# Kernel optimization log

Measured on AMD Instinct MI355X. Metric: run time of the kernel, lower is better.

The kernel has to match this reference:

```python
import jax, jax.numpy as jnp
import numpy as np

H = W = 512
P = H * W          # total superpixel member pixels
N_SP = 1024        # number of superpixels


def _conv(x, w, b):
    # x: [N,C,H,W], w: [O,I,3,3] -> [N,O,H,W], SAME padding
    y = jax.lax.conv_general_dilated(
        x, w, window_strides=(1, 1), padding='SAME',
        dimension_numbers=('NCHW', 'OIHW', 'NCHW'))
    return y + b[None, :, None, None]


def _embed(raw, w1, b1, w2, b2, w3, b3):
    h = jax.nn.relu(_conv(raw, w1, b1))
    h = jax.nn.relu(_conv(h, w2, b2))
    return _conv(h, w3, b3)  # [1, 10, H, W]


def setup_inputs() -> dict:
    key = jax.random.key(0)
    ks = jax.random.split(key, 6)
    raw = jax.random.normal(ks[0], (1, 1, H, W), dtype=jnp.float32)
    w1 = jax.random.normal(ks[1], (64, 1, 3, 3), dtype=jnp.float32) * 0.3
    b1 = jnp.zeros((64,), jnp.float32)
    w2 = jax.random.normal(ks[2], (64, 64, 3, 3), dtype=jnp.float32) * 0.05
    b2 = jnp.zeros((64,), jnp.float32)
    w3 = jax.random.normal(ks[3], (10, 64, 3, 3), dtype=jnp.float32) * 0.05
    b3 = jnp.zeros((10,), jnp.float32)
    pix_rc = jax.random.randint(ks[4], (P, 2), 0, H, dtype=jnp.int32)
    seg_ids = jax.random.randint(ks[5], (P,), 0, N_SP, dtype=jnp.int32)
    return {"raw": raw, "w1": w1, "b1": b1, "w2": w2, "b2": b2,
            "w3": w3, "b3": b3, "pix_rc": pix_rc, "seg_ids": seg_ids,
            "n_sp": N_SP}


def reference(raw, w1, b1, w2, b2, w3, b3, pix_rc, seg_ids, n_sp):
    feats = _embed(raw, w1, b1, w2, b2, w3, b3)  # [1, C, H, W]
    f = feats[0]                                  # [C, H, W]
    # gather per-pixel feature vectors: [P, C]
    vals = f[:, pix_rc[:, 0], pix_rc[:, 1]].T
    # scatter-mean over superpixels (= per-sp sum / mass)
    sums = jax.ops.segment_sum(vals, seg_ids, num_segments=n_sp)      # [n_sp, C]
    cnts = jax.ops.segment_sum(jnp.ones((vals.shape[0],), vals.dtype),
                               seg_ids, num_segments=n_sp)            # [n_sp]
    return sums / jnp.maximum(cnts, 1.0)[:, None]
```

## Files before the change

kernel.cpp:

```cpp
#include <hip/hip_runtime.h>

typedef __attribute__((ext_vector_type(8))) short short8;
typedef __attribute__((ext_vector_type(4))) float f32x4;

constexpr int H = 512, W = 512;
constexpr int P = H * W;
constexpr int NSP = 1024;
constexpr int SBLK = 512;
constexpr int FGRP = 16;

__device__ inline unsigned short f2bf(float f) {
  unsigned u = __builtin_bit_cast(unsigned, f);
  unsigned r = (u + 0x7fffu + ((u >> 16) & 1u)) >> 16;
  return (unsigned short)r;
}
__device__ inline float bflo(unsigned u) { return __builtin_bit_cast(float, u << 16); }
__device__ inline float bfhi(unsigned u) { return __builtin_bit_cast(float, u & 0xffff0000u); }

__device__ inline int xcd_swz(int b, int cpx) { return (b & 7) * cpx + (b >> 3); }

__global__ __launch_bounds__(256) void prep_k(const float* __restrict__ w2,
                                              const float* __restrict__ w3,
                                              unsigned short* __restrict__ wt2s,
                                              unsigned short* __restrict__ wt3s) {
  int i = blockIdx.x * 256 + threadIdx.x;
  if (i < 36864) {
    int k = i >> 11;
    int t = (i >> 3) & 255;
    int e = i & 7;
    int r = t >> 2, sp = t & 3, s = sp ^ (r & 3);
    int tap = k >> 1, ic = (k & 1) * 32 + s * 8 + e;
    wt2s[i] = f2bf(w2[r * 576 + ic * 9 + tap]);
  } else if (i < 46080) {
    int j = i - 36864;
    int k = j >> 9;
    int t = (j >> 3) & 63;
    int e = j & 7;
    int r = t >> 2, sp = t & 3, s = sp ^ (r & 3);
    int tap = k >> 1, ic = (k & 1) * 32 + s * 8 + e;
    wt3s[j] = (r < 10) ? f2bf(w3[r * 576 + ic * 9 + tap]) : (unsigned short)0;
  }
}

__global__ __launch_bounds__(512, 4) void conv123_k(const float* __restrict__ raw,
                                                    const float* __restrict__ w1,
                                                    const float* __restrict__ b1,
                                                    const unsigned short* __restrict__ wts2,
                                                    const float* __restrict__ b2,
                                                    const unsigned short* __restrict__ wts3,
                                                    const float* __restrict__ b3,
                                                    unsigned short* __restrict__ feats) {
  constexpr int WCS = 2048;
  __shared__ __align__(16) unsigned short acts[448 * 64];
  __shared__ __align__(16) unsigned short wbuf[3 * WCS];
  __shared__ float rawt[14 * 38];
  int tid = threadIdx.x;
  int lane = tid & 63, wave = tid >> 6;
  int logical = xcd_swz(blockIdx.x, 128);
  int tilex = logical & 15, tiley = logical >> 4;
  int c0 = tilex * 32, r0 = tiley * 8;

  if (tid < 256) {
#pragma unroll
    for (int k0 = 0; k0 < 2; ++k0) {
      const unsigned short* src = wts2 + (size_t)k0 * WCS + tid * 8;
      unsigned short* dstb = wbuf + k0 * WCS + wave * 512;
      __builtin_amdgcn_global_load_lds((const __attribute__((address_space(1))) void*)src,
                                       (__attribute__((address_space(3))) void*)dstb, 16, 0, 0);
    }
  }
  for (int i = tid; i < 532; i += 512) {
    int rr = i / 38, cc = i - rr * 38;
    int gr = r0 + rr - 3, gc = c0 + cc - 3;
    bool ok = ((unsigned)gr < 512u) && ((unsigned)gc < 512u);
    rawt[i] = ok ? raw[gr * 512 + gc] : 0.f;
  }

  int q = lane >> 4, n = lane & 15;
  int og1 = wave & 3;
  short8 a1f;
  {
    short av[8];
#pragma unroll
    for (int e = 0; e < 8; ++e) av[e] = 0;
    int oc = og1 * 16 + n;
    if (q == 0) {
#pragma unroll
      for (int e = 0; e < 8; ++e) av[e] = (short)f2bf(w1[oc * 9 + e]);
    } else if (q == 1) {
      av[0] = (short)f2bf(w1[oc * 9 + 8]);
    }
    a1f = (short8){av[0], av[1], av[2], av[3], av[4], av[5], av[6], av[7]};
  }
  float bb1[4];
#pragma unroll
  for (int r2 = 0; r2 < 4; ++r2) bb1[r2] = b1[og1 * 16 + q * 4 + r2];
  __syncthreads();

  char* actw = (char*)acts;
  int hhalf = wave >> 2;
  for (int i1 = 0; i1 < 14; ++i1) {
    int t = 2 * i1 + hhalf;
    if (t >= 27) break;
    int px = t * 16 + n;
    int py = px / 36, pxc = px - py * 36;
    short bv[8];
#pragma unroll
    for (int e = 0; e < 8; ++e) bv[e] = 0;
    if (q == 0) {
#pragma unroll
      for (int e = 0; e < 8; ++e) {
        int dy = e / 3, dx = e - dy * 3;
        bv[e] = (short)f2bf(rawt[(py + dy) * 38 + pxc + dx]);
      }
    } else if (q == 1) {
      bv[0] = (short)f2bf(rawt[(py + 2) * 38 + pxc + 2]);
    }
    short8 b1f = (short8){bv[0], bv[1], bv[2], bv[3], bv[4], bv[5], bv[6], bv[7]};
    f32x4 d = __builtin_amdgcn_mfma_f32_16x16x32_bf16(a1f, b1f,
                                                       (f32x4){0.f, 0.f, 0.f, 0.f}, 0, 0, 0);
    int gr1 = r0 + py - 2, gc1 = c0 + pxc - 2;
    bool ok1 = ((unsigned)gr1 < 512u) && ((unsigned)gc1 < 512u);
    float o0 = ok1 ? fmaxf(d.x + bb1[0], 0.f) : 0.f;
    float o1 = ok1 ? fmaxf(d.y + bb1[1], 0.f) : 0.f;
    float o2 = ok1 ? fmaxf(d.z + bb1[2], 0.f) : 0.f;
    float o3 = ok1 ? fmaxf(d.w + bb1[3], 0.f) : 0.f;
    unsigned lo = (unsigned)f2bf(o0) | ((unsigned)f2bf(o1) << 16);
    unsigned hi = (unsigned)f2bf(o2) | ((unsigned)f2bf(o3) << 16);
    int wa = px * 128 + ((((og1 * 2 + (q >> 1)) ^ (px & 7)) << 4)) + ((q & 1) << 3);
    *reinterpret_cast<uint2*>(actw + wa) = make_uint2(lo, hi);
  }
  __syncthreads();

  f32x4 acc[4][3];
#pragma unroll
  for (int og = 0; og < 4; ++og)
#pragma unroll
    for (int g = 0; g < 3; ++g) acc[og][g] = (f32x4){0.f, 0.f, 0.f, 0.f};
  const char* actb = (const char*)acts;

#pragma unroll
  for (int k = 0; k < 18; ++k) {
    if (k == 17) {
      asm volatile("s_waitcnt vmcnt(0)" ::: "memory");
    } else {
      asm volatile("s_waitcnt vmcnt(1)" ::: "memory");
    }
    __builtin_amdgcn_sched_barrier(0);
    __builtin_amdgcn_s_barrier();
    __builtin_amdgcn_sched_barrier(0);
    if (k + 2 < 18 && tid < 256) {
      const unsigned short* src = wts2 + (size_t)(k + 2) * WCS + tid * 8;
      unsigned short* dstb = wbuf + ((k + 2) % 3) * WCS + wave * 512;
      __builtin_amdgcn_global_load_lds((const __attribute__((address_space(1))) void*)src,
                                       (__attribute__((address_space(3))) void*)dstb, 16, 0, 0);
    }
    const int tap = k >> 1, kc = k & 1;
    const int kyy = tap / 3, kxx = tap - kyy * 3;
    const char* wb = (const char*)(wbuf + (k % 3) * WCS);
    short8 af[4];
#pragma unroll
    for (int og = 0; og < 4; ++og) {
      int r = og * 16 + n;
      af[og] = *reinterpret_cast<const short8*>(wb + r * 64 + ((q ^ (r & 3)) * 16));
    }
#pragma unroll
    for (int g = 0; g < 3; ++g) {
      int t2 = wave + 8 * g;
      if (t2 < 23) {
        int pl = t2 * 16 + n + kyy * 36 + kxx;
        int addr = pl * 128 + (((kc * 4 + q) ^ (pl & 7)) * 16);
        short8 bf = *reinterpret_cast<const short8*>(actb + addr);
#pragma unroll
        for (int og = 0; og < 4; ++og)
          acc[og][g] = __builtin_amdgcn_mfma_f32_16x16x32_bf16(af[og], bf, acc[og][g], 0, 0, 0);
      }
    }
  }
  __syncthreads();

  if (tid < 64) {
#pragma unroll
    for (int k0 = 0; k0 < 2; ++k0) {
      const unsigned short* src = wts3 + (size_t)k0 * 512 + lane * 8;
      unsigned short* dstb = &wbuf[k0 * 512];
      __builtin_amdgcn_global_load_lds((const __attribute__((address_space(1))) void*)src,
                                       (__attribute__((address_space(3))) void*)dstb, 16, 0, 0);
    }
  }
#pragma unroll
  for (int g = 0; g < 3; ++g) {
    int t2 = wave + 8 * g;
    if (t2 < 23) {
      int px2 = t2 * 16 + n;
#pragma unroll
      for (int og = 0; og < 4; ++og) {
        f32x4 v = acc[og][g];
        float o0 = fmaxf(v.x + b2[og * 16 + q * 4 + 0], 0.f);
        float o1 = fmaxf(v.y + b2[og * 16 + q * 4 + 1], 0.f);
        float o2 = fmaxf(v.z + b2[og * 16 + q * 4 + 2], 0.f);
        float o3 = fmaxf(v.w + b2[og * 16 + q * 4 + 3], 0.f);
        unsigned lo = (unsigned)f2bf(o0) | ((unsigned)f2bf(o1) << 16);
        unsigned hi = (unsigned)f2bf(o2) | ((unsigned)f2bf(o3) << 16);
        int lslot = og * 2 + (q >> 1);
        int wa = px2 * 128 + (((lslot ^ (px2 & 7)) << 4)) + ((q & 1) << 3);
        *reinterpret_cast<uint2*>(actw + wa) = make_uint2(lo, hi);
      }
    }
  }
  __syncthreads();

  f32x4 acc3[2];
#pragma unroll
  for (int g = 0; g < 2; ++g) acc3[g] = (f32x4){0.f, 0.f, 0.f, 0.f};
  const char* wb3 = (const char*)wbuf;

#pragma unroll
  for (int k = 0; k < 18; ++k) {
    if (k == 17) {
      asm volatile("s_waitcnt vmcnt(0)" ::: "memory");
    } else {
      asm volatile("s_waitcnt vmcnt(1)" ::: "memory");
    }
    __builtin_amdgcn_sched_barrier(0);
    __builtin_amdgcn_s_barrier();
    __builtin_amdgcn_sched_barrier(0);
    if (k + 2 < 18 && tid < 64) {
      const unsigned short* src = wts3 + (size_t)(k + 2) * 512 + lane * 8;
      unsigned short* dstb = &wbuf[((k + 2) % 3) * 512];
      __builtin_amdgcn_global_load_lds((const __attribute__((address_space(1))) void*)src,
                                       (__attribute__((address_space(3))) void*)dstb, 16, 0, 0);
    }
    const int tap = k >> 1, kc = k & 1;
    const int kyy = tap / 3, kxx = tap - kyy * 3;
    short8 af = *reinterpret_cast<const short8*>(wb3 + (k % 3) * 1024 + n * 64 + ((q ^ (n & 3)) * 16));
#pragma unroll
    for (int g = 0; g < 2; ++g) {
      int pl = wave * 36 + g * 16 + n + kyy * 36 + kxx;
      int addr = pl * 128 + (((kc * 4 + q) ^ (pl & 7)) * 16);
      short8 bf = *reinterpret_cast<const short8*>(actb + addr);
      acc3[g] = __builtin_amdgcn_mfma_f32_16x16x32_bf16(af, bf, acc3[g], 0, 0, 0);
    }
  }

  __syncthreads();
  char* ob = (char*)acts;
  float bb3[4];
#pragma unroll
  for (int r2 = 0; r2 < 4; ++r2) {
    int oc = q * 4 + r2;
    bb3[r2] = (oc < 10) ? b3[oc] : 0.f;
  }
#pragma unroll
  for (int g = 0; g < 2; ++g) {
    int pl = wave * 32 + g * 16 + n;
    f32x4 v = acc3[g];
    float o0 = v.x + bb3[0], o1 = v.y + bb3[1], o2 = v.z + bb3[2], o3 = v.w + bb3[3];
    if (q < 2) {
      unsigned u0 = (unsigned)f2bf(o0) | ((unsigned)f2bf(o1) << 16);
      unsigned u1 = (unsigned)f2bf(o2) | ((unsigned)f2bf(o3) << 16);
      *reinterpret_cast<uint2*>(ob + pl * 24 + q * 8) = make_uint2(u0, u1);
    } else if (q == 2) {
      *reinterpret_cast<unsigned*>(ob + pl * 24 + 16) =
          (unsigned)f2bf(o0) | ((unsigned)f2bf(o1) << 16);
    }
  }
  __syncthreads();
  char* fb = (char*)feats;
#pragma unroll
  for (int it = 0; it < 3; ++it) {
    int c = it * 512 + tid;
    if (c < 1280) {
      int row = c / 160, wb = c - row * 160;
      int byte = wb * 4;
      int px = byte / 20, off = byte - px * 20;
      unsigned v = *reinterpret_cast<const unsigned*>(ob + (row * 32 + px) * 24 + off);
      size_t gbyte = (((size_t)(r0 + row) * 512) + c0) * 20 + (size_t)byte;
      *reinterpret_cast<unsigned*>(fb + gbyte) = v;
    }
  }
}

__global__ __launch_bounds__(512) void scatter_k(const unsigned short* __restrict__ feats,
                                                 const int* __restrict__ pix_rc,
                                                 const int* __restrict__ seg,
                                                 float* __restrict__ partials) {
  __shared__ float ls[NSP * 10];
  __shared__ float lc[NSP];
  int tid = threadIdx.x;
  for (int i = tid; i < NSP * 10; i += 512) ls[i] = 0.f;
  for (int i = tid; i < NSP; i += 512) lc[i] = 0.f;
  __syncthreads();

  constexpr int PER = P / SBLK;
  int p0 = blockIdx.x * PER;
  for (int p = p0 + tid; p < p0 + PER; p += 512) {
    int r = pix_rc[2 * p], c = pix_rc[2 * p + 1];
    int s = seg[p];
    size_t gpix = (size_t)r * 512 + c;
    const char* fp = (const char*)feats + gpix * 20;
    uint4 a = *reinterpret_cast<const uint4*>(fp);
    unsigned e = *reinterpret_cast<const unsigned*>(fp + 16);
    float v[10];
    v[0] = bflo(a.x); v[1] = bfhi(a.x);
    v[2] = bflo(a.y); v[3] = bfhi(a.y);
    v[4] = bflo(a.z); v[5] = bfhi(a.z);
    v[6] = bflo(a.w); v[7] = bfhi(a.w);
    v[8] = bflo(e);   v[9] = bfhi(e);
#pragma unroll
    for (int ch = 0; ch < 10; ++ch) atomicAdd(&ls[s * 10 + ch], v[ch]);
    atomicAdd(&lc[s], 1.f);
  }
  __syncthreads();

  float* outp = partials + (size_t)blockIdx.x * (NSP * 11);
  for (int i = tid; i < NSP * 10; i += 512) outp[i] = ls[i];
  for (int i = tid; i < NSP; i += 512) outp[NSP * 10 + i] = lc[i];
}

__global__ __launch_bounds__(256) void finA_k(const float* __restrict__ partials,
                                              float* __restrict__ partials2) {
  int g = blockIdx.x / 44;
  int e = (blockIdx.x - g * 44) * 256 + threadIdx.x;
  const float* base = partials + (size_t)(g * 32) * (NSP * 11) + e;
  float s = 0.f;
#pragma unroll 8
  for (int k = 0; k < 32; ++k) s += base[(size_t)k * (NSP * 11)];
  partials2[(size_t)g * (NSP * 11) + e] = s;
}

__global__ __launch_bounds__(256) void finB_k(const float* __restrict__ partials2,
                                              float* __restrict__ out) {
  int i = blockIdx.x * 256 + threadIdx.x;
  if (i >= NSP * 10) return;
  int sp = i / 10;
  float s = 0.f, cnt = 0.f;
#pragma unroll
  for (int g = 0; g < FGRP; ++g) {
    const float* pp = partials2 + (size_t)g * (NSP * 11);
    s += pp[i];
    cnt += pp[NSP * 10 + sp];
  }
  out[i] = s / fmaxf(cnt, 1.f);
}

extern "C" void kernel_launch(void* const* d_in, const int* in_sizes, int n_in,
                              void* d_out, int out_size, void* d_ws, size_t ws_size,
                              hipStream_t stream) {
  const float* raw = (const float*)d_in[0];
  const float* w1  = (const float*)d_in[1];
  const float* b1  = (const float*)d_in[2];
  const float* w2  = (const float*)d_in[3];
  const float* b2  = (const float*)d_in[4];
  const float* w3  = (const float*)d_in[5];
  const float* b3  = (const float*)d_in[6];
  const int* pix_rc = (const int*)d_in[7];
  const int* seg    = (const int*)d_in[8];
  float* out = (float*)d_out;

  char* ws = (char*)d_ws;
  float* partials  = (float*)(ws + 0);
  float* partials2 = (float*)(ws + 23068672);
  unsigned short* feats = (unsigned short*)(ws + 25165824);
  unsigned short* wt2s = (unsigned short*)(ws + 30408704);
  unsigned short* wt3s = (unsigned short*)(ws + 30482432);

  prep_k<<<180, 256, 0, stream>>>(w2, w3, wt2s, wt3s);
  conv123_k<<<1024, 512, 0, stream>>>(raw, w1, b1, wt2s, b2, wt3s, b3, feats);
  scatter_k<<<SBLK, 512, 0, stream>>>(feats, pix_rc, seg, partials);
  finA_k<<<FGRP * 44, 256, 0, stream>>>(partials, partials2);
  finB_k<<<40, 256, 0, stream>>>(partials2, out);
}
```

Baseline: 85.21 us.

## Deepen conv2 weight prefetch, preload all conv3 weights, use bf16 raw tile

The conv2 weight ring grows from three to four LDS slots, so each chunk is prefetched three steps ahead with looser vmcnt waits. All eighteen conv3 weight chunks are now loaded into LDS up front by every wave, which removes the per-step waitcnt and barrier from the conv3 loop. The raw input tile is converted to bf16 once when staged, instead of on every read. The weight swizzle key changes from r&3 to (r>>2)&3 to spread LDS bank accesses. In exchange LDS use grows somewhat, and the conv3 loop now relies on the preceding __syncthreads to make sure the async loads have landed.

```diff
diff --git a/kernel.cpp b/kernel.cpp
--- a/kernel.cpp
+++ b/kernel.cpp
@@ -28,7 +28,7 @@
     int k = i >> 11;
     int t = (i >> 3) & 255;
     int e = i & 7;
-    int r = t >> 2, sp = t & 3, s = sp ^ (r & 3);
+    int r = t >> 2, sp = t & 3, s = sp ^ ((r >> 2) & 3);
     int tap = k >> 1, ic = (k & 1) * 32 + s * 8 + e;
     wt2s[i] = f2bf(w2[r * 576 + ic * 9 + tap]);
   } else if (i < 46080) {
@@ -36,7 +36,7 @@
     int k = j >> 9;
     int t = (j >> 3) & 63;
     int e = j & 7;
-    int r = t >> 2, sp = t & 3, s = sp ^ (r & 3);
+    int r = t >> 2, sp = t & 3, s = sp ^ ((r >> 2) & 3);
     int tap = k >> 1, ic = (k & 1) * 32 + s * 8 + e;
     wt3s[j] = (r < 10) ? f2bf(w3[r * 576 + ic * 9 + tap]) : (unsigned short)0;
   }
@@ -52,8 +52,8 @@
                                                     unsigned short* __restrict__ feats) {
   constexpr int WCS = 2048;
   __shared__ __align__(16) unsigned short acts[448 * 64];
-  __shared__ __align__(16) unsigned short wbuf[3 * WCS];
-  __shared__ float rawt[14 * 38];
+  __shared__ __align__(16) unsigned short wbuf[9216];
+  __shared__ unsigned short rawtb[14 * 38 + 12];
   int tid = threadIdx.x;
   int lane = tid & 63, wave = tid >> 6;
   int logical = xcd_swz(blockIdx.x, 128);
@@ -62,9 +62,9 @@
 
   if (tid < 256) {
 #pragma unroll
-    for (int k0 = 0; k0 < 2; ++k0) {
+    for (int k0 = 0; k0 < 3; ++k0) {
       const unsigned short* src = wts2 + (size_t)k0 * WCS + tid * 8;
-      unsigned short* dstb = wbuf + k0 * WCS + wave * 512;
+      unsigned short* dstb = wbuf + (k0 & 3) * WCS + wave * 512;
       __builtin_amdgcn_global_load_lds((const __attribute__((address_space(1))) void*)src,
                                        (__attribute__((address_space(3))) void*)dstb, 16, 0, 0);
     }
@@ -73,7 +73,7 @@
     int rr = i / 38, cc = i - rr * 38;
     int gr = r0 + rr - 3, gc = c0 + cc - 3;
     bool ok = ((unsigned)gr < 512u) && ((unsigned)gc < 512u);
-    rawt[i] = ok ? raw[gr * 512 + gc] : 0.f;
+    rawtb[i] = ok ? f2bf(raw[gr * 512 + gc]) : (unsigned short)0;
   }
 
   int q = lane >> 4, n = lane & 15;
@@ -111,10 +111,10 @@
 #pragma unroll
       for (int e = 0; e < 8; ++e) {
         int dy = e / 3, dx = e - dy * 3;
-        bv[e] = (short)f2bf(rawt[(py + dy) * 38 + pxc + dx]);
+        bv[e] = (short)rawtb[(py + dy) * 38 + pxc + dx];
       }
     } else if (q == 1) {
-      bv[0] = (short)f2bf(rawt[(py + 2) * 38 + pxc + 2]);
+      bv[0] = (short)rawtb[(py + 2) * 38 + pxc + 2];
     }
     short8 b1f = (short8){bv[0], bv[1], bv[2], bv[3], bv[4], bv[5], bv[6], bv[7]};
     f32x4 d = __builtin_amdgcn_mfma_f32_16x16x32_bf16(a1f, b1f,
@@ -143,26 +143,28 @@
   for (int k = 0; k < 18; ++k) {
     if (k == 17) {
       asm volatile("s_waitcnt vmcnt(0)" ::: "memory");
+    } else if (k == 16) {
+      asm volatile("s_waitcnt vmcnt(1)" ::: "memory");
     } else {
-      asm volatile("s_waitcnt vmcnt(1)" ::: "memory");
+      asm volatile("s_waitcnt vmcnt(2)" ::: "memory");
     }
     __builtin_amdgcn_sched_barrier(0);
     __builtin_amdgcn_s_barrier();
     __builtin_amdgcn_sched_barrier(0);
-    if (k + 2 < 18 && tid < 256) {
-      const unsigned short* src = wts2 + (size_t)(k + 2) * WCS + tid * 8;
-      unsigned short* dstb = wbuf + ((k + 2) % 3) * WCS + wave * 512;
+    if (k + 3 < 18 && tid < 256) {
+      const unsigned short* src = wts2 + (size_t)(k + 3) * WCS + tid * 8;
+      unsigned short* dstb = wbuf + ((k + 3) & 3) * WCS + wave * 512;
       __builtin_amdgcn_global_load_lds((const __attribute__((address_space(1))) void*)src,
                                        (__attribute__((address_space(3))) void*)dstb, 16, 0, 0);
     }
     const int tap = k >> 1, kc = k & 1;
     const int kyy = tap / 3, kxx = tap - kyy * 3;
-    const char* wb = (const char*)(wbuf + (k % 3) * WCS);
+    const char* wb = (const char*)(wbuf + (k & 3) * WCS);
     short8 af[4];
 #pragma unroll
     for (int og = 0; og < 4; ++og) {
       int r = og * 16 + n;
-      af[og] = *reinterpret_cast<const short8*>(wb + r * 64 + ((q ^ (r & 3)) * 16));
+      af[og] = *reinterpret_cast<const short8*>(wb + r * 64 + ((q ^ ((r >> 2) & 3)) * 16));
     }
 #pragma unroll
     for (int g = 0; g < 3; ++g) {
@@ -179,14 +181,11 @@
   }
   __syncthreads();
 
-  if (tid < 64) {
-#pragma unroll
-    for (int k0 = 0; k0 < 2; ++k0) {
-      const unsigned short* src = wts3 + (size_t)k0 * 512 + lane * 8;
-      unsigned short* dstb = &wbuf[k0 * 512];
-      __builtin_amdgcn_global_load_lds((const __attribute__((address_space(1))) void*)src,
-                                       (__attribute__((address_space(3))) void*)dstb, 16, 0, 0);
-    }
+  for (int wi = wave; wi < 18; wi += 8) {
+    const unsigned short* src = wts3 + (size_t)wi * 512 + lane * 8;
+    unsigned short* dstb = &wbuf[wi * 512];
+    __builtin_amdgcn_global_load_lds((const __attribute__((address_space(1))) void*)src,
+                                     (__attribute__((address_space(3))) void*)dstb, 16, 0, 0);
   }
 #pragma unroll
   for (int g = 0; g < 3; ++g) {
@@ -217,23 +216,10 @@
 
 #pragma unroll
   for (int k = 0; k < 18; ++k) {
-    if (k == 17) {
-      asm volatile("s_waitcnt vmcnt(0)" ::: "memory");
-    } else {
-      asm volatile("s_waitcnt vmcnt(1)" ::: "memory");
-    }
-    __builtin_amdgcn_sched_barrier(0);
-    __builtin_amdgcn_s_barrier();
-    __builtin_amdgcn_sched_barrier(0);
-    if (k + 2 < 18 && tid < 64) {
-      const unsigned short* src = wts3 + (size_t)(k + 2) * 512 + lane * 8;
-      unsigned short* dstb = &wbuf[((k + 2) % 3) * 512];
-      __builtin_amdgcn_global_load_lds((const __attribute__((address_space(1))) void*)src,
-                                       (__attribute__((address_space(3))) void*)dstb, 16, 0, 0);
-    }
     const int tap = k >> 1, kc = k & 1;
     const int kyy = tap / 3, kxx = tap - kyy * 3;
-    short8 af = *reinterpret_cast<const short8*>(wb3 + (k % 3) * 1024 + n * 64 + ((q ^ (n & 3)) * 16));
+    short8 af = *reinterpret_cast<const short8*>(wb3 + k * 1024 + n * 64 +
+                                                 ((q ^ ((n >> 2) & 3)) * 16));
 #pragma unroll
     for (int g = 0; g < 2; ++g) {
       int pl = wave * 36 + g * 16 + n + kyy * 36 + kxx;
```

After: 83.27 us. -2.3%, faster.
